# Performance work log

Measured on AMD Instinct MI355X. Metric: run time of the kernel, lower is better.

## Reference

```python
import jax, jax.numpy as jnp
import numpy as np

B = 8192
C, S1, S2 = 3, 64, 64
F = C * S1 * S2          # 12288 flattened input features
SU = 4096                # s_units
HID = 1024               # hidden_size
NL = 4                   # s_layers
D = 8                    # num_domains
H1, H2, NW = 28, 14, 5   # omniglot head dims, num_ways
BN_EPS = 1e-5
LEAK = 0.001


def setup_inputs() -> dict:
    key = jax.random.key(0)
    ks = jax.random.split(key, 24)
    sc = 0.02
    n = lambda k, shp: (jax.random.normal(k, shp, jnp.float32) * sc)
    return {
        'x_s': jax.random.normal(ks[0], (B, C, S1, S2), jnp.float32),
        'x_p': jax.random.normal(ks[1], (B, C, S1, S2), jnp.float32),
        'tt': jax.random.randint(ks[2], (B,), 0, D),
        'domain_id': 3,
        # Shared MLP
        'W_in': n(ks[3], (F, SU)),  'b_in': jnp.zeros((SU,), jnp.float32),
        'W_hid': n(ks[4], (SU, SU)), 'b_hid': jnp.zeros((SU,), jnp.float32),
        'W_out': n(ks[5], (SU, HID)), 'b_out': jnp.zeros((HID,), jnp.float32),
        # Private per-domain linear (stacked)
        'Wp': n(ks[6], (D, F, HID)), 'bp': jnp.zeros((D, HID), jnp.float32),
        # BatchNorm1d affine params
        'gamma': jnp.ones((2 * HID,), jnp.float32),
        'beta': jnp.zeros((2 * HID,), jnp.float32),
        # Per-domain head MLPs (stacked)
        'Wh1': n(ks[7], (D, 2 * HID, H1)), 'bh1': jnp.zeros((D, H1), jnp.float32),
        'Wh2': n(ks[8], (D, H1, H2)),      'bh2': jnp.zeros((D, H2), jnp.float32),
        'Wh3': n(ks[9], (D, H2, NW)),      'bh3': jnp.zeros((D, NW), jnp.float32),
    }


def _forward(x_s, x_p, tt, domain_id, W_in, b_in, W_hid, b_hid, W_out, b_out,
             Wp, bp, gamma, beta, Wh1, bh1, Wh2, bh2, Wh3, bh3):
    b = x_s.shape[0]
    hs = x_s.reshape(b, -1)
    hp = x_p.reshape(b, -1)

    # Shared branch (dropout = identity in eval)
    h = jax.nn.relu(hs @ W_in + b_in)
    for _ in range(NL):
        h = jax.nn.relu(h @ W_hid + b_hid)
    h_shared = jax.nn.relu(h @ W_out + b_out)

    # Private branch: single domain-selected linear + LeakyReLU(0.001)
    h_priv = jax.nn.leaky_relu(hp @ Wp[domain_id] + bp[domain_id], LEAK)

    x = jnp.concatenate([h_shared, h_priv], axis=1)  # [B, 2*HID]

    # BatchNorm1d (training-mode batch statistics, biased variance)
    mean = jnp.mean(x, axis=0)
    var = jnp.var(x, axis=0)
    x = (x - mean) * jax.lax.rsqrt(var + BN_EPS) * gamma + beta

    # Per-sample task-routed heads: gather weights by tt, batched GEMMs
    y = jax.nn.relu(jnp.einsum('bf,bfo->bo', x, Wh1[tt]) + bh1[tt])
    y = jax.nn.relu(jnp.einsum('bf,bfo->bo', y, Wh2[tt]) + bh2[tt])
    y = jnp.einsum('bf,bfo->bo', y, Wh3[tt]) + bh3[tt]
    return y  # [B, num_ways]


def reference(x_s, x_p, tt, domain_id, W_in, b_in, W_hid, b_hid, W_out, b_out,
              Wp, bp, gamma, beta, Wh1, bh1, Wh2, bh2, Wh3, bh3):
    return _forward(x_s, x_p, tt, domain_id, W_in, b_in, W_hid, b_hid,
                    W_out, b_out, Wp, bp, gamma, beta,
                    Wh1, bh1, Wh2, bh2, Wh3, bh3)
```

## Files before the change

kernel.cpp:

```cpp
#include <hip/hip_runtime.h>
#include <hip/hip_bf16.h>

#define BQ    8192
#define FIN   12288
#define SUN   4096
#define HIDN  1024
#define XW    2048
#define H1N   28
#define H2N   14
#define NWAY  5
#define BN_EPS 1e-5f
#define LEAKS 0.001f

typedef __bf16 bf16x8 __attribute__((ext_vector_type(8)));
typedef float  f32x4  __attribute__((ext_vector_type(4)));
typedef unsigned short ushort8 __attribute__((ext_vector_type(8)));

__device__ __forceinline__ unsigned short f2bf(float f) {
    unsigned u = __float_as_uint(f);
    unsigned r = u + 0x7fffu + ((u >> 16) & 1u);
    return (unsigned short)(r >> 16);
}

__device__ __forceinline__ ushort8 cvt8(const float4 a, const float4 b) {
    union { __bf16 h[8]; ushort8 u; } r;
    r.h[0] = (__bf16)a.x; r.h[1] = (__bf16)a.y;
    r.h[2] = (__bf16)a.z; r.h[3] = (__bf16)a.w;
    r.h[4] = (__bf16)b.x; r.h[5] = (__bf16)b.y;
    r.h[6] = (__bf16)b.z; r.h[7] = (__bf16)b.w;
    return r.u;
}

#define TO_LDS(p) ((__attribute__((address_space(3))) void*)(p))
#define TO_GLB(p) ((const __attribute__((address_space(1))) void*)(p))


__global__ __launch_bounds__(256) void cvt_bf16(
    const float* __restrict__ in, unsigned short* __restrict__ out, long long n8)
{
    const long long idx = (long long)blockIdx.x * 256 + threadIdx.x;
    const long long stride = (long long)gridDim.x * 256;
    for (long long i = idx; i < n8; i += stride) {
        const float4 a = ((const float4*)in)[2 * i];
        const float4 b = ((const float4*)in)[2 * i + 1];
        ((ushort8*)out)[i] = cvt8(a, b);
    }
}

__global__ __launch_bounds__(256) void transpose_cvt(
    const float* __restrict__ in, unsigned short* __restrict__ out,
    int R, int Cc, const int* __restrict__ dom)
{
    if (dom) in += (size_t)(*dom) * (size_t)R * (size_t)Cc;
    __shared__ float tile[64][65];
    const int t  = threadIdx.x;
    const int tr = t >> 4;
    const int tc = t & 15;
    const int c0 = blockIdx.x * 64;
    const int r0 = blockIdx.y * 64;

    #pragma unroll
    for (int q = 0; q < 4; ++q) {
        const int r = r0 + tr + q * 16;
        const float4 v = *(const float4*)&in[(size_t)r * Cc + c0 + tc * 4];
        tile[tc*4+0][tr + q*16] = v.x;
        tile[tc*4+1][tr + q*16] = v.y;
        tile[tc*4+2][tr + q*16] = v.z;
        tile[tc*4+3][tr + q*16] = v.w;
    }
    __syncthreads();
    #pragma unroll
    for (int q = 0; q < 4; ++q) {
        const int c = c0 + tr + q * 16;
        ushort4 o;
        o.x = f2bf(tile[tr + q*16][tc*4+0]);
        o.y = f2bf(tile[tr + q*16][tc*4+1]);
        o.z = f2bf(tile[tr + q*16][tc*4+2]);
        o.w = f2bf(tile[tr + q*16][tc*4+3]);
        *(ushort4*)&out[(size_t)c * R + r0 + tc * 4] = o;
    }
}

template<bool A_F32, bool OUT_F32, int ACT>
__global__ __launch_bounds__(256) void gemm_mfma(
    const void* __restrict__ Ap, const unsigned short* __restrict__ Bt,
    const float* __restrict__ bias, void* __restrict__ Cp,
    int M, int N, int K, int ldc, int cc0,
    const int* __restrict__ dom, int biasStride)
{
    __shared__ alignas(16) unsigned short As[128 * 32];
    __shared__ alignas(16) unsigned short Bs[128 * 32];

    const int nbx = N >> 7;
    int wg = blockIdx.x;
    const int nwg = gridDim.x;
    if ((nwg & 7) == 0) {
        const int cpx = nwg >> 3;
        wg = (wg & 7) * cpx + (wg >> 3);
    }
    const int bx = wg % nbx, by = wg / nbx;
    const int row0 = by << 7, col0 = bx << 7;

    const int t  = threadIdx.x;
    const int w  = t >> 6;
    const int l  = t & 63;
    const int wr = w >> 1, wc = w & 1;
    const int lr = l & 15, lk = l >> 4;
    const int rsw = (lr >> 1) & 3;

    f32x4 acc[4][4];
    #pragma unroll
    for (int i = 0; i < 4; ++i)
        #pragma unroll
        for (int j = 0; j < 4; ++j)
            acc[i][j] = (f32x4)(0.f);

    const int srow = l >> 2;
    const int skb  = (((l & 3) ^ ((l >> 3) & 3)) * 16);
    const float* Af = (const float*)Ap;
    const unsigned short* Ab = (const unsigned short*)Ap;

    for (int k0 = 0; k0 < K; k0 += 32) {
        __syncthreads();

        #pragma unroll
        for (int c = 0; c < 2; ++c) {
            const int inst = w * 2 + c;
            const int row  = inst * 16 + srow;
            const char* src = (const char*)Bt +
                (((size_t)(col0 + row) * K + k0) * 2 + skb);
            char* dst = (char*)Bs + inst * 1024;
            __builtin_amdgcn_global_load_lds(TO_GLB(src), TO_LDS(dst), 16, 0, 0);
        }
        if (!A_F32) {
            #pragma unroll
            for (int c = 0; c < 2; ++c) {
                const int inst = w * 2 + c;
                const int row  = inst * 16 + srow;
                const char* src = (const char*)Ab +
                    (((size_t)(row0 + row) * K + k0) * 2 + skb);
                char* dst = (char*)As + inst * 1024;
                __builtin_amdgcn_global_load_lds(TO_GLB(src), TO_LDS(dst), 16, 0, 0);
            }
        } else {
            #pragma unroll
            for (int c = 0; c < 2; ++c) {
                const int ci  = t + 256 * c;
                const int row = ci >> 2;
                const int ko  = (((ci & 3) ^ ((ci >> 3) & 3)) * 8);
                const float* s = Af + (size_t)(row0 + row) * K + k0 + ko;
                const float4 v0 = *(const float4*)s;
                const float4 v1 = *(const float4*)(s + 4);
                *(ushort8*)&As[ci * 8] = cvt8(v0, v1);
            }
        }
        __syncthreads();

        bf16x8 af[4], bfv[4];
        #pragma unroll
        for (int i = 0; i < 4; ++i)
            af[i]  = *(const bf16x8*)&As[(wr*64 + i*16 + lr) * 32 + (lk ^ rsw) * 8];
        #pragma unroll
        for (int j = 0; j < 4; ++j)
            bfv[j] = *(const bf16x8*)&Bs[(wc*64 + j*16 + lr) * 32 + (lk ^ rsw) * 8];
        #pragma unroll
        for (int i = 0; i < 4; ++i)
            #pragma unroll
            for (int j = 0; j < 4; ++j)
                acc[i][j] = __builtin_amdgcn_mfma_f32_16x16x32_bf16(
                    af[i], bfv[j], acc[i][j], 0, 0, 0);
    }

    if (dom) bias += (*dom) * biasStride;
    const int colb = col0 + wc * 64 + lr;
    const int rowb = row0 + wr * 64 + lk * 4;
    float bj[4];
    #pragma unroll
    for (int j = 0; j < 4; ++j) bj[j] = bias[colb + j * 16];

    #pragma unroll
    for (int i = 0; i < 4; ++i) {
        #pragma unroll
        for (int r = 0; r < 4; ++r) {
            const size_t row = rowb + i * 16 + r;
            #pragma unroll
            for (int j = 0; j < 4; ++j) {
                float x = acc[i][j][r] + bj[j];
                if (ACT == 1)      x = fmaxf(x, 0.f);
                else if (ACT == 2) x = (x > 0.f) ? x : LEAKS * x;
                const size_t idx = row * (size_t)ldc + cc0 + colb + j * 16;
                if (OUT_F32) ((float*)Cp)[idx] = x;
                else         ((unsigned short*)Cp)[idx] = f2bf(x);
            }
        }
    }
}

__global__ __launch_bounds__(512, 2) void gemm256(
    const unsigned short* __restrict__ A, const unsigned short* __restrict__ Bt,
    const float* __restrict__ bias, unsigned short* __restrict__ C,
    int M, int N, int K)
{
    __shared__ alignas(16) unsigned short lds[3][2][256 * 32];

    const int nbx = N >> 8;
    int wg = blockIdx.x;
    const int nwg = gridDim.x;
    if ((nwg & 7) == 0) {
        const int cpx = nwg >> 3;
        wg = (wg & 7) * cpx + (wg >> 3);
    }
    const int bx = wg % nbx, by = wg / nbx;
    const int row0 = by << 8, col0 = bx << 8;

    const int t  = threadIdx.x;
    const int w  = t >> 6, l = t & 63;
    const int wr = w >> 2, wc = w & 3;
    const int lr = l & 15, lk = l >> 4;
    const int rsw = (lr >> 1) & 3;
    const int srow = l >> 2;
    const int skel = ((l & 3) ^ ((l >> 3) & 3)) * 8;

    f32x4 acc[8][4];
    #pragma unroll
    for (int i = 0; i < 8; ++i)
        #pragma unroll
        for (int j = 0; j < 4; ++j)
            acc[i][j] = (f32x4)(0.f);

    const int NT = K >> 5;

    #define STAGE256(tile_)  do {                                            \
        const int k0_  = (tile_) << 5;                                       \
        const int buf_ = (tile_) % 3;                                        \
        _Pragma("unroll")                                                    \
        for (int s_ = 0; s_ < 2; ++s_) {                                     \
            const int c_   = w * 2 + s_;                                     \
            const int row_ = c_ * 16 + srow;                                 \
            __builtin_amdgcn_global_load_lds(                                \
                TO_GLB(A + (size_t)(row0 + row_) * K + k0_ + skel),          \
                TO_LDS((char*)&lds[buf_][0][0] + c_ * 1024), 16, 0, 0);      \
            __builtin_amdgcn_global_load_lds(                                \
                TO_GLB(Bt + (size_t)(col0 + row_) * K + k0_ + skel),         \
                TO_LDS((char*)&lds[buf_][1][0] + c_ * 1024), 16, 0, 0);      \
        }                                                                    \
    } while (0)

    STAGE256(0);
    if (NT > 1) {
        STAGE256(1);
        asm volatile("s_waitcnt vmcnt(4)" ::: "memory");
    } else {
        asm volatile("s_waitcnt vmcnt(0)" ::: "memory");
    }
    __builtin_amdgcn_sched_barrier(0);
    __builtin_amdgcn_s_barrier();
    __builtin_amdgcn_sched_barrier(0);

    for (int tt = 0; tt < NT; ++tt) {
        const int buf = tt % 3;
        if (tt + 2 < NT) STAGE256(tt + 2);
        __builtin_amdgcn_sched_barrier(0);

        bf16x8 af[8], bfv[4];
        #pragma unroll
        for (int i = 0; i < 8; ++i)
            af[i]  = *(const bf16x8*)&lds[buf][0][(wr*128 + i*16 + lr) * 32 + (lk ^ rsw) * 8];
        #pragma unroll
        for (int j = 0; j < 4; ++j)
            bfv[j] = *(const bf16x8*)&lds[buf][1][(wc*64 + j*16 + lr) * 32 + (lk ^ rsw) * 8];

        #pragma unroll
        for (int j = 0; j < 4; ++j)
            #pragma unroll
            for (int i = 0; i < 8; ++i)
                acc[i][j] = __builtin_amdgcn_mfma_f32_16x16x32_bf16(
                    af[i], bfv[j], acc[i][j], 0, 0, 0);

        if (tt + 1 < NT) {
            if (tt + 2 < NT) asm volatile("s_waitcnt vmcnt(4)" ::: "memory");
            else             asm volatile("s_waitcnt vmcnt(0)" ::: "memory");
            __builtin_amdgcn_sched_barrier(0);
            __builtin_amdgcn_s_barrier();
            __builtin_amdgcn_sched_barrier(0);
        }
    }
    #undef STAGE256

    const int colb = col0 + wc * 64 + lr;
    const int rowb = row0 + wr * 128 + lk * 4;
    float bj[4];
    #pragma unroll
    for (int j = 0; j < 4; ++j) bj[j] = bias[colb + j * 16];

    #pragma unroll
    for (int i = 0; i < 8; ++i) {
        #pragma unroll
        for (int r = 0; r < 4; ++r) {
            const size_t row = rowb + i * 16 + r;
            #pragma unroll
            for (int j = 0; j < 4; ++j) {
                float x = fmaxf(acc[i][j][r] + bj[j], 0.f);
                C[row * (size_t)N + colb + j * 16] = f2bf(x);
            }
        }
    }
}

__global__ __launch_bounds__(256) void bn_stats_a(
    const float* __restrict__ X, float* __restrict__ psum, float* __restrict__ pss)
{
    const int c  = blockIdx.x * 256 + threadIdx.x;
    const int rb = blockIdx.y;
    float s = 0.f, ss = 0.f;
    const int r0 = rb * 256;
    for (int r = r0; r < r0 + 256; ++r) {
        float v = X[(size_t)r * XW + c];
        s += v; ss = fmaf(v, v, ss);
    }
    psum[rb * XW + c] = s;
    pss [rb * XW + c] = ss;
}

__global__ __launch_bounds__(256) void bn_stats_b(
    const float* __restrict__ psum, const float* __restrict__ pss,
    const float* __restrict__ gamma, const float* __restrict__ beta,
    float* __restrict__ scale, float* __restrict__ shift)
{
    const int c = blockIdx.x * 256 + threadIdx.x;
    float s = 0.f, ss = 0.f;
    for (int rb = 0; rb < 32; ++rb) { s += psum[rb * XW + c]; ss += pss[rb * XW + c]; }
    const float inv = 1.f / (float)BQ;
    const float mean = s * inv;
    const float var  = ss * inv - mean * mean;
    const float sc = gamma[c] * rsqrtf(var + BN_EPS);
    scale[c] = sc;
    shift[c] = beta[c] - mean * sc;
}

__global__ __launch_bounds__(256) void head_kernel(
    const float* __restrict__ X, const float* __restrict__ scale,
    const float* __restrict__ shift, const int* __restrict__ tt,
    const float* __restrict__ Wh1, const float* __restrict__ bh1,
    const float* __restrict__ Wh2, const float* __restrict__ bh2,
    const float* __restrict__ Wh3, const float* __restrict__ bh3,
    float* __restrict__ out)
{
    __shared__ float xs[4][XW];
    __shared__ float y1[4][H1N];
    __shared__ float y2[4][H2N + 2];

    const int t = threadIdx.x;
    const int w = t >> 6;
    const int l = t & 63;
    const int s = blockIdx.x * 4 + w;
    const int d = tt[s];

    #pragma unroll 4
    for (int i = 0; i < XW / 64; ++i) {
        const int c = i * 64 + l;
        xs[w][c] = fmaf(X[(size_t)s * XW + c], scale[c], shift[c]);
    }
    __syncthreads();

    if (l < H1N) {
        const float* W1 = Wh1 + (size_t)d * XW * H1N;
        float acc = bh1[d * H1N + l];
        #pragma unroll 8
        for (int c = 0; c < XW; ++c)
            acc = fmaf(xs[w][c], W1[c * H1N + l], acc);
        y1[w][l] = fmaxf(acc, 0.f);
    }
    __syncthreads();

    if (l < H2N) {
        const float* W2 = Wh2 + (size_t)d * H1N * H2N;
        float acc = bh2[d * H2N + l];
        #pragma unroll
        for (int c = 0; c < H1N; ++c)
            acc = fmaf(y1[w][c], W2[c * H2N + l], acc);
        y2[w][l] = fmaxf(acc, 0.f);
    }
    __syncthreads();

    if (l < NWAY) {
        const float* W3 = Wh3 + (size_t)d * H2N * NWAY;
        float acc = bh3[d * NWAY + l];
        #pragma unroll
        for (int c = 0; c < H2N; ++c)
            acc = fmaf(y2[w][c], W3[c * NWAY + l], acc);
        out[(size_t)s * NWAY + l] = acc;
    }
}

extern "C" void kernel_launch(void* const* d_in, const int* in_sizes, int n_in,
                              void* d_out, int out_size, void* d_ws, size_t ws_size,
                              hipStream_t stream)
{
    const float* x_s   = (const float*)d_in[0];
    const float* x_p   = (const float*)d_in[1];
    const int*   tt    = (const int*)  d_in[2];
    const int*   dom   = (const int*)  d_in[3];
    const float* W_in  = (const float*)d_in[4];
    const float* b_in  = (const float*)d_in[5];
    const float* W_hid = (const float*)d_in[6];
    const float* b_hid = (const float*)d_in[7];
    const float* W_out = (const float*)d_in[8];
    const float* b_out = (const float*)d_in[9];
    const float* Wp    = (const float*)d_in[10];
    const float* bp    = (const float*)d_in[11];
    const float* gamma = (const float*)d_in[12];
    const float* beta  = (const float*)d_in[13];
    const float* Wh1   = (const float*)d_in[14];
    const float* bh1   = (const float*)d_in[15];
    const float* Wh2   = (const float*)d_in[16];
    const float* bh2   = (const float*)d_in[17];
    const float* Wh3   = (const float*)d_in[18];
    const float* bh3   = (const float*)d_in[19];
    float* out = (float*)d_out;

    const dim3 blk(256);
    char* w = (char*)d_ws;

    const size_t FAST_NEED = 470810624ull;

    if (ws_size >= FAST_NEED) {
        unsigned short* xb    = (unsigned short*)w;
        unsigned short* WinT  = (unsigned short*)(w + 201326592);
        unsigned short* WoutT = (unsigned short*)(w + 201326592);
        unsigned short* WpT   = (unsigned short*)(w + 209715200);
        unsigned short* actA  = (unsigned short*)(w + 301989888);
        unsigned short* actB  = (unsigned short*)(w + 369098752);
        float*          X     = (float*)(w + 369098752);
        unsigned short* WhidT = (unsigned short*)(w + 436207616);
        float*          psum  = (float*)(w + 469762048);
        float*          pss   = psum + 32 * XW;
        float*          scale = pss  + 32 * XW;
        float*          shift = scale + XW;

        cvt_bf16<<<dim3(2048), blk, 0, stream>>>(x_s, xb, (long long)BQ * FIN / 8);
        transpose_cvt<<<dim3(SUN/64,  FIN/64), blk, 0, stream>>>(W_in,  WinT,  FIN, SUN,  nullptr);
        transpose_cvt<<<dim3(SUN/64,  SUN/64), blk, 0, stream>>>(W_hid, WhidT, SUN, SUN,  nullptr);

        gemm256<<<dim3(512), dim3(512), 0, stream>>>(xb, WinT, b_in, actA, BQ, SUN, FIN);

        transpose_cvt<<<dim3(HIDN/64, SUN/64), blk, 0, stream>>>(W_out, WoutT, SUN, HIDN, nullptr);
        transpose_cvt<<<dim3(HIDN/64, FIN/64), blk, 0, stream>>>(Wp,    WpT,   FIN, HIDN, dom);
        cvt_bf16<<<dim3(2048), blk, 0, stream>>>(x_p, xb, (long long)BQ * FIN / 8);

        gemm256<<<dim3(512), dim3(512), 0, stream>>>(actA, WhidT, b_hid, actB, BQ, SUN, SUN);
        gemm256<<<dim3(512), dim3(512), 0, stream>>>(actB, WhidT, b_hid, actA, BQ, SUN, SUN);
        gemm256<<<dim3(512), dim3(512), 0, stream>>>(actA, WhidT, b_hid, actB, BQ, SUN, SUN);
        gemm256<<<dim3(512), dim3(512), 0, stream>>>(actB, WhidT, b_hid, actA, BQ, SUN, SUN);

        gemm_mfma<false,true,1><<<dim3(512), blk, 0, stream>>>(
            actA, WoutT, b_out, X, BQ, HIDN, SUN, XW, 0, nullptr, 0);
        gemm_mfma<false,true,2><<<dim3(512), blk, 0, stream>>>(
            xb, WpT, bp, X, BQ, HIDN, FIN, XW, HIDN, dom, HIDN);

        bn_stats_a<<<dim3(XW/256, 32), blk, 0, stream>>>(X, psum, pss);
        bn_stats_b<<<dim3(XW/256),     blk, 0, stream>>>(psum, pss, gamma, beta, scale, shift);
        head_kernel<<<dim3(BQ/4), blk, 0, stream>>>(X, scale, shift, tt,
                                                    Wh1, bh1, Wh2, bh2, Wh3, bh3, out);
        return;
    }

    unsigned short* actA  = (unsigned short*)w;
    unsigned short* actB  = (unsigned short*)(w + 67108864);
    float*          X     = (float*)(w + 67108864);
    unsigned short* WinT  = (unsigned short*)(w + 134217728);
    unsigned short* WoutT = (unsigned short*)(w + 134217728);
    unsigned short* WpT   = (unsigned short*)(w + 142606336);
    float*          psum  = (float*)(w + 167772160);
    float*          pss   = psum + 32 * XW;
    float*          scale = pss  + 32 * XW;
    float*          shift = scale + XW;
    unsigned short* WhidT = (unsigned short*)(w + 234881024);

    transpose_cvt<<<dim3(SUN/64,  FIN/64), blk, 0, stream>>>(W_in,  WinT,  FIN, SUN,  nullptr);
    transpose_cvt<<<dim3(SUN/64,  SUN/64), blk, 0, stream>>>(W_hid, WhidT, SUN, SUN,  nullptr);

    gemm_mfma<true,false,1><<<dim3(2048), blk, 0, stream>>>(
        x_s, WinT, b_in, actA, BQ, SUN, FIN, SUN, 0, nullptr, 0);

    transpose_cvt<<<dim3(HIDN/64, SUN/64), blk, 0, stream>>>(W_out, WoutT, SUN, HIDN, nullptr);
    transpose_cvt<<<dim3(HIDN/64, FIN/64), blk, 0, stream>>>(Wp,    WpT,   FIN, HIDN, dom);

    gemm256<<<dim3(512), dim3(512), 0, stream>>>(actA, WhidT, b_hid, actB, BQ, SUN, SUN);
    gemm256<<<dim3(512), dim3(512), 0, stream>>>(actB, WhidT, b_hid, actA, BQ, SUN, SUN);
    gemm256<<<dim3(512), dim3(512), 0, stream>>>(actA, WhidT, b_hid, actB, BQ, SUN, SUN);
    gemm256<<<dim3(512), dim3(512), 0, stream>>>(actB, WhidT, b_hid, actA, BQ, SUN, SUN);

    gemm_mfma<false,true,1><<<dim3(512), blk, 0, stream>>>(
        actA, WoutT, b_out, X, BQ, HIDN, SUN, XW, 0, nullptr, 0);
    gemm_mfma<true,true,2><<<dim3(512), blk, 0, stream>>>(
        x_p, WpT, bp, X, BQ, HIDN, FIN, XW, HIDN, dom, HIDN);

    bn_stats_a<<<dim3(XW/256, 32), blk, 0, stream>>>(X, psum, pss);
    bn_stats_b<<<dim3(XW/256),     blk, 0, stream>>>(psum, pss, gamma, beta, scale, shift);
    head_kernel<<<dim3(BQ/4), blk, 0, stream>>>(X, scale, shift, tt,
                                                Wh1, bh1, Wh2, bh2, Wh3, bh3, out);
}
```

Before: 2.619 ms.

## Add triple-buffered direct-to-LDS 128x128 GEMM for output and private layers

Adds a new gemm128 kernel that uses global_load_lds into a three-stage LDS ring with swizzled rows and an XCD-aware workgroup remap. It replaces gemm_mfma for the W_out GEMM on both paths and for the private Wp GEMM on the pre-converted path. The aim is better overlap of global loads with MFMA work on these narrower GEMMs. It also raises wave priority around the MFMA block in gemm256, which may change how waves are scheduled against loads.

```diff
diff --git a/kernel.cpp b/kernel.cpp
--- a/kernel.cpp
+++ b/kernel.cpp
@@ -270,12 +270,14 @@
         for (int j = 0; j < 4; ++j)
             bfv[j] = *(const bf16x8*)&lds[buf][1][(wc*64 + j*16 + lr) * 32 + (lk ^ rsw) * 8];
 
+        __builtin_amdgcn_s_setprio(1);
         #pragma unroll
         for (int j = 0; j < 4; ++j)
             #pragma unroll
             for (int i = 0; i < 8; ++i)
                 acc[i][j] = __builtin_amdgcn_mfma_f32_16x16x32_bf16(
                     af[i], bfv[j], acc[i][j], 0, 0, 0);
+        __builtin_amdgcn_s_setprio(0);
 
         if (tt + 1 < NT) {
             if (tt + 2 < NT) asm volatile("s_waitcnt vmcnt(4)" ::: "memory");
@@ -302,6 +304,124 @@
             for (int j = 0; j < 4; ++j) {
                 float x = fmaxf(acc[i][j][r] + bj[j], 0.f);
                 C[row * (size_t)N + colb + j * 16] = f2bf(x);
+            }
+        }
+    }
+}
+
+template<bool OUT_F32, int ACT>
+__global__ __launch_bounds__(256, 2) void gemm128(
+    const unsigned short* __restrict__ A, const unsigned short* __restrict__ Bt,
+    const float* __restrict__ bias, void* __restrict__ Cp,
+    int M, int N, int K, int ldc, int cc0,
+    const int* __restrict__ dom, int biasStride)
+{
+    __shared__ alignas(16) unsigned short lds[3][2][128 * 32];
+
+    const int nbx = N >> 7;
+    int wg = blockIdx.x;
+    const int nwg = gridDim.x;
+    if ((nwg & 7) == 0) {
+        const int cpx = nwg >> 3;
+        wg = (wg & 7) * cpx + (wg >> 3);
+    }
+    const int bx = wg % nbx, by = wg / nbx;
+    const int row0 = by << 7, col0 = bx << 7;
+
+    const int t  = threadIdx.x;
+    const int w  = t >> 6, l = t & 63;
+    const int wr = w >> 1, wc = w & 1;
+    const int lr = l & 15, lk = l >> 4;
+    const int rsw = (lr >> 1) & 3;
+    const int srow = l >> 2;
+    const int skel = ((l & 3) ^ ((l >> 3) & 3)) * 8;
+
+    f32x4 acc[4][4];
+    #pragma unroll
+    for (int i = 0; i < 4; ++i)
+        #pragma unroll
+        for (int j = 0; j < 4; ++j)
+            acc[i][j] = (f32x4)(0.f);
+
+    const int NT = K >> 5;
+
+    #define STAGE128(tile_)  do {                                            \
+        const int k0_  = (tile_) << 5;                                       \
+        const int buf_ = (tile_) % 3;                                        \
+        _Pragma("unroll")                                                    \
+        for (int s_ = 0; s_ < 2; ++s_) {                                     \
+            const int c_   = w * 2 + s_;                                     \
+            const int row_ = c_ * 16 + srow;                                 \
+            __builtin_amdgcn_global_load_lds(                                \
+                TO_GLB(A + (size_t)(row0 + row_) * K + k0_ + skel),          \
+                TO_LDS((char*)&lds[buf_][0][0] + c_ * 1024), 16, 0, 0);      \
+            __builtin_amdgcn_global_load_lds(                                \
+                TO_GLB(Bt + (size_t)(col0 + row_) * K + k0_ + skel),         \
+                TO_LDS((char*)&lds[buf_][1][0] + c_ * 1024), 16, 0, 0);      \
+        }                                                                    \
+    } while (0)
+
+    STAGE128(0);
+    if (NT > 1) {
+        STAGE128(1);
+        asm volatile("s_waitcnt vmcnt(4)" ::: "memory");
+    } else {
+        asm volatile("s_waitcnt vmcnt(0)" ::: "memory");
+    }
+    __builtin_amdgcn_sched_barrier(0);
+    __builtin_amdgcn_s_barrier();
+    __builtin_amdgcn_sched_barrier(0);
+
+    for (int tt = 0; tt < NT; ++tt) {
+        const int buf = tt % 3;
+        if (tt + 2 < NT) STAGE128(tt + 2);
+        __builtin_amdgcn_sched_barrier(0);
+
+        bf16x8 af[4], bfv[4];
+        #pragma unroll
+        for (int i = 0; i < 4; ++i)
+            af[i]  = *(const bf16x8*)&lds[buf][0][(wr*64 + i*16 + lr) * 32 + (lk ^ rsw) * 8];
+        #pragma unroll
+        for (int j = 0; j < 4; ++j)
+            bfv[j] = *(const bf16x8*)&lds[buf][1][(wc*64 + j*16 + lr) * 32 + (lk ^ rsw) * 8];
+
+        #pragma unroll
+        for (int j = 0; j < 4; ++j)
+            #pragma unroll
+            for (int i = 0; i < 4; ++i)
+                acc[i][j] = __builtin_amdgcn_mfma_f32_16x16x32_bf16(
+                    af[i], bfv[j], acc[i][j], 0, 0, 0);
+
+        if (tt + 1 < NT) {
+            if (tt + 2 < NT) asm volatile("s_waitcnt vmcnt(4)" ::: "memory");
+            else             asm volatile("s_waitcnt vmcnt(0)" ::: "memory");
+            __builtin_amdgcn_sched_barrier(0);
+            __builtin_amdgcn_s_barrier();
+            __builtin_amdgcn_sched_barrier(0);
+        }
+    }
+    #undef STAGE128
+
+    if (dom) bias += (*dom) * biasStride;
+    const int colb = col0 + wc * 64 + lr;
+    const int rowb = row0 + wr * 64 + lk * 4;
+    float bj[4];
+    #pragma unroll
+    for (int j = 0; j < 4; ++j) bj[j] = bias[colb + j * 16];
+
+    #pragma unroll
+    for (int i = 0; i < 4; ++i) {
+        #pragma unroll
+        for (int r = 0; r < 4; ++r) {
+            const size_t row = rowb + i * 16 + r;
+            #pragma unroll
+            for (int j = 0; j < 4; ++j) {
+                float x = acc[i][j][r] + bj[j];
+                if (ACT == 1)      x = fmaxf(x, 0.f);
+                else if (ACT == 2) x = (x > 0.f) ? x : LEAKS * x;
+                const size_t idx = row * (size_t)ldc + cc0 + colb + j * 16;
+                if (OUT_F32) ((float*)Cp)[idx] = x;
+                else         ((unsigned short*)Cp)[idx] = f2bf(x);
             }
         }
     }
@@ -453,9 +573,9 @@
         gemm256<<<dim3(512), dim3(512), 0, stream>>>(actA, WhidT, b_hid, actB, BQ, SUN, SUN);
         gemm256<<<dim3(512), dim3(512), 0, stream>>>(actB, WhidT, b_hid, actA, BQ, SUN, SUN);
 
-        gemm_mfma<false,true,1><<<dim3(512), blk, 0, stream>>>(
+        gemm128<true,1><<<dim3(512), blk, 0, stream>>>(
             actA, WoutT, b_out, X, BQ, HIDN, SUN, XW, 0, nullptr, 0);
-        gemm_mfma<false,true,2><<<dim3(512), blk, 0, stream>>>(
+        gemm128<true,2><<<dim3(512), blk, 0, stream>>>(
             xb, WpT, bp, X, BQ, HIDN, FIN, XW, HIDN, dom, HIDN);
 
         bn_stats_a<<<dim3(XW/256, 32), blk, 0, stream>>>(X, psum, pss);
@@ -491,7 +611,7 @@
     gemm256<<<dim3(512), dim3(512), 0, stream>>>(actA, WhidT, b_hid, actB, BQ, SUN, SUN);
     gemm256<<<dim3(512), dim3(512), 0, stream>>>(actB, WhidT, b_hid, actA, BQ, SUN, SUN);
 
-    gemm_mfma<false,true,1><<<dim3(512), blk, 0, stream>>>(
+    gemm128<true,1><<<dim3(512), blk, 0, stream>>>(
         actA, WoutT, b_out, X, BQ, HIDN, SUN, XW, 0, nullptr, 0);
     gemm_mfma<true,true,2><<<dim3(512), blk, 0, stream>>>(
         x_p, WpT, bp, X, BQ, HIDN, FIN, XW, HIDN, dom, HIDN);
```

Result: faster. 2.521 ms (-3.8%).
